# Performance work log

Measured on AMD Instinct MI355X. Metric: run time of the kernel, lower is better.

Reference implementation:

```python
import jax, jax.numpy as jnp
import numpy as np

B, N, EMB, H = 16, 1024, 128, 8
INNER = EMB * H  # 1024
EPS = 1e-5


def setup_inputs() -> dict:
    key = jax.random.key(0)
    k1, k2, k3 = jax.random.split(key, 3)
    inputs = jax.random.normal(k1, (B, N, EMB), dtype=jnp.float32)
    ln_gamma = jnp.ones((EMB,), dtype=jnp.float32)
    ln_beta = jnp.zeros((EMB,), dtype=jnp.float32)
    w_qkv = jax.random.normal(k2, (EMB, 3 * INNER), dtype=jnp.float32) * (EMB ** -0.5)
    w_proj = jax.random.normal(k3, (INNER, EMB), dtype=jnp.float32) * (INNER ** -0.5)
    b_proj = jnp.zeros((EMB,), dtype=jnp.float32)
    return {"inputs": inputs, "ln_gamma": ln_gamma, "ln_beta": ln_beta,
            "w_qkv": w_qkv, "w_proj": w_proj, "b_proj": b_proj}


def reference(inputs, ln_gamma, ln_beta, w_qkv, w_proj, b_proj):
    scale = INNER ** -0.5
    # LayerNorm over last dim
    mu = jnp.mean(inputs, axis=-1, keepdims=True)
    var = jnp.var(inputs, axis=-1, keepdims=True)
    x = (inputs - mu) * jax.lax.rsqrt(var + EPS) * ln_gamma + ln_beta
    # QKV projection (no bias)
    qkv = x @ w_qkv                                  # [b, n, 3*inner]
    q, k, v = jnp.split(qkv, 3, axis=-1)             # each [b, n, inner]
    def to_heads(a):
        return a.reshape(B, N, H, EMB).transpose(0, 2, 1, 3)  # [b, h, n, d]
    q, k, v = to_heads(q), to_heads(k), to_heads(v)
    attn = jnp.einsum('bhid,bhjd->bhij', q * scale, k)
    attn = jax.nn.softmax(attn, axis=-1)
    out = jnp.einsum('bhij,bhjd->bhid', attn, v)     # [b, h, n, d]
    out = out.transpose(0, 2, 1, 3).reshape(B, N, INNER)
    return out @ w_proj + b_proj                     # [b, n, emb]
```

## Files before the change

kernel.cpp:

```cpp
#include <hip/hip_runtime.h>
#include <hip/hip_bf16.h>


typedef __attribute__((ext_vector_type(8))) short bf16x8;
typedef __attribute__((ext_vector_type(4))) float f32x4;

__device__ __forceinline__ unsigned short f2bf(float f) {
  unsigned int u = __float_as_uint(f);
  u += 0x7FFF + ((u >> 16) & 1);
  return (unsigned short)(u >> 16);
}

__device__ __forceinline__ void gll16(const void* g, void* l) {
  __builtin_amdgcn_global_load_lds((const __attribute__((address_space(1))) unsigned int*)g,
                                   (__attribute__((address_space(3))) unsigned int*)l, 16, 0, 0);
}

__global__ __launch_bounds__(256) void k_ln(const float* __restrict__ x,
                                            const float* __restrict__ gamma,
                                            const float* __restrict__ beta,
                                            unsigned short* __restrict__ xb) {
  int row  = blockIdx.x * 4 + (threadIdx.x >> 6);
  int lane = threadIdx.x & 63;
  float2 v = *reinterpret_cast<const float2*>(x + row * 128 + lane * 2);
  float s = v.x + v.y, ss = v.x * v.x + v.y * v.y;
#pragma unroll
  for (int m = 1; m < 64; m <<= 1) { s += __shfl_xor(s, m); ss += __shfl_xor(ss, m); }
  float mu   = s * (1.0f / 128.0f);
  float var  = ss * (1.0f / 128.0f) - mu * mu;
  float rstd = rsqrtf(var + 1e-5f);
  float2 g  = *reinterpret_cast<const float2*>(gamma + lane * 2);
  float2 be = *reinterpret_cast<const float2*>(beta + lane * 2);
  ushort2 o;
  o.x = f2bf((v.x - mu) * rstd * g.x + be.x);
  o.y = f2bf((v.y - mu) * rstd * g.y + be.y);
  *reinterpret_cast<ushort2*>(xb + row * 128 + lane * 2) = o;
}

__global__ __launch_bounds__(256) void k_cast_wqkv(const float* __restrict__ w,
                                                   unsigned short* __restrict__ wt) {
  __shared__ unsigned short T[128][70];
  const int n0 = blockIdx.x * 64;
  const int tid = threadIdx.x;
#pragma unroll
  for (int i = 0; i < 32; i++) {
    int idx = i * 256 + tid;
    int k = idx >> 6, c = idx & 63;
    T[k][c] = f2bf(w[k * 3072 + n0 + c]);
  }
  __syncthreads();
#pragma unroll
  for (int i = 0; i < 32; i++) {
    int idx = i * 256 + tid;
    int n = idx >> 7, k = idx & 127;
    wt[(n0 + n) * 128 + k] = T[k][n];
  }
}

__global__ __launch_bounds__(256) void k_cast_wproj(const float* __restrict__ w,
                                                    unsigned short* __restrict__ wt) {
  __shared__ unsigned short T[128][134];
  const int k0 = blockIdx.x * 128;
  const int tid = threadIdx.x;
#pragma unroll
  for (int i = 0; i < 64; i++) {
    int idx = i * 256 + tid;
    int r = idx >> 7, c = idx & 127;
    T[r][c] = f2bf(w[(k0 + r) * 128 + c]);
  }
  __syncthreads();
#pragma unroll
  for (int i = 0; i < 64; i++) {
    int idx = i * 256 + tid;
    int c = idx >> 7, r = idx & 127;
    wt[c * 1024 + k0 + r] = T[r][c];
  }
}

__global__ __launch_bounds__(256) void k_qkv(const unsigned short* __restrict__ xb,
                                             const unsigned short* __restrict__ wt,
                                             unsigned short* __restrict__ qb,
                                             unsigned short* __restrict__ kb,
                                             unsigned short* __restrict__ vtb) {
  __shared__ __align__(16) unsigned short Xs[128][128];
  __shared__ __align__(16) unsigned short Ws[128][128];
  const int m0 = blockIdx.x * 128;
  const int n0 = blockIdx.y * 128;
  const int tid = threadIdx.x, wave = tid >> 6, lane = tid & 63;
  const int lm = lane & 15, lg = lane >> 4;
  const int wr = wave >> 1, wc = wave & 1;

#pragma unroll
  for (int ii = 0; ii < 8; ii++) {
    int row = wave * 32 + ii * 4 + (lane >> 4);
    int c = (lane & 15) ^ (row & 7);
    gll16(xb + (m0 + row) * 128 + c * 8, &Xs[wave * 32 + ii * 4][0]);
    gll16(wt + (n0 + row) * 128 + c * 8, &Ws[wave * 32 + ii * 4][0]);
  }
  __syncthreads();

  f32x4 acc[4][4];
#pragma unroll
  for (int i = 0; i < 4; i++)
#pragma unroll
    for (int j = 0; j < 4; j++) acc[i][j] = {0.f, 0.f, 0.f, 0.f};

#pragma unroll
  for (int k32 = 0; k32 < 4; k32++) {
    bf16x8 af[4], bfr[4];
#pragma unroll
    for (int mi = 0; mi < 4; mi++) {
      int row = wr * 64 + mi * 16 + lm;
      af[mi] = *(const bf16x8*)((const char*)&Xs[row][0] + ((k32 * 64 + lg * 16) ^ ((lm & 7) << 4)));
    }
#pragma unroll
    for (int ni = 0; ni < 4; ni++) {
      int row = wc * 64 + ni * 16 + lm;
      bfr[ni] = *(const bf16x8*)((const char*)&Ws[row][0] + ((k32 * 64 + lg * 16) ^ ((lm & 7) << 4)));
    }
#pragma unroll
    for (int mi = 0; mi < 4; mi++)
#pragma unroll
      for (int ni = 0; ni < 4; ni++)
        acc[mi][ni] = __builtin_amdgcn_mfma_f32_16x16x32_bf16(af[mi], bfr[ni], acc[mi][ni], 0, 0, 0);
  }

#pragma unroll
  for (int mi = 0; mi < 4; mi++)
#pragma unroll
    for (int ni = 0; ni < 4; ni++)
#pragma unroll
      for (int j = 0; j < 4; j++) {
        int m = m0 + wr * 64 + mi * 16 + 4 * (lane >> 4) + j;
        int n = n0 + wc * 64 + ni * 16 + lm;
        float val = acc[mi][ni][j];
        int bb = m >> 10, seq = m & 1023;
        int sel = n >> 10, r = n & 1023, h = r >> 7, d = r & 127;
        int bh = bb * 8 + h;
        if (sel == 0)      qb[(bh * 1024 + seq) * 128 + d] = f2bf(val * 0.04508422f);
        else if (sel == 1) kb[(bh * 1024 + seq) * 128 + d] = f2bf(val);
        else               vtb[(bh * 128 + d) * 1024 + seq] = f2bf(val);
      }
}

__global__ __launch_bounds__(256, 3) void k_flash(const unsigned short* __restrict__ qb,
                                                  const unsigned short* __restrict__ kb,
                                                  const unsigned short* __restrict__ vtb,
                                                  unsigned short* __restrict__ ob) {
  __shared__ __align__(16) unsigned short Ks[64][128];
  __shared__ __align__(16) unsigned short Vts[128][64];
  __shared__ __align__(16) unsigned short Ps[4][32][64];
  const int bi = blockIdx.x;
  const int xcd = bi & 7, g = bi >> 3;
  const int bh = xcd + 8 * (g >> 3);
  const int q0 = (g & 7) * 128;
  const int tid = threadIdx.x, wave = tid >> 6, lane = tid & 63;
  const int lm = lane & 15, lg = lane >> 4, lk8 = lg * 8;
  const int sw = (lm & 7) << 4;
  const int b = bh >> 3, h = bh & 7;

  const unsigned short* kbh = kb + bh * 131072;
  const unsigned short* vbh = vtb + bh * 131072;

  bf16x8 aq[2][4];
#pragma unroll
  for (int qs = 0; qs < 2; qs++) {
    const unsigned short* qrow = qb + (bh * 1024 + q0 + wave * 32 + qs * 16 + lm) * 128;
#pragma unroll
    for (int kc = 0; kc < 4; kc++) aq[qs][kc] = *(const bf16x8*)(qrow + kc * 32 + lk8);
  }

  f32x4 oacc[2][8];
#pragma unroll
  for (int qs = 0; qs < 2; qs++)
#pragma unroll
    for (int dt = 0; dt < 8; dt++) oacc[qs][dt] = {0.f, 0.f, 0.f, 0.f};
  float mrun[2] = {-3e38f, -3e38f}, lrun[2] = {0.f, 0.f};

  auto stage = [&](int kt) {
#pragma unroll
    for (int ii = 0; ii < 4; ii++) {
      int krow = (wave * 4 + ii) * 4 + (lane >> 4);
      int c = (lane & 15) ^ (krow & 7);
      gll16(kbh + (kt * 64 + krow) * 128 + c * 8, &Ks[(wave * 4 + ii) * 4][0]);
    }
#pragma unroll
    for (int ii = 0; ii < 4; ii++) {
      int vrow = (wave * 4 + ii) * 8 + (lane >> 3);
      int c = (lane & 7) ^ (vrow & 7);
      gll16(vbh + vrow * 1024 + kt * 64 + c * 8, &Vts[(wave * 4 + ii) * 8][0]);
    }
  };

  stage(0);
  __syncthreads();

  for (int kt = 0; kt < 16; kt++) {
    f32x4 sc[2][4];
    __builtin_amdgcn_s_setprio(1);
#pragma unroll
    for (int nt = 0; nt < 4; nt++) {
      f32x4 a0 = {0.f, 0.f, 0.f, 0.f}, a1 = {0.f, 0.f, 0.f, 0.f};
      const char* krowp = (const char*)&Ks[nt * 16 + lm][0];
#pragma unroll
      for (int kc = 0; kc < 4; kc++) {
        bf16x8 ak = *(const bf16x8*)(krowp + ((kc * 64 + lg * 16) ^ sw));
        a0 = __builtin_amdgcn_mfma_f32_16x16x32_bf16(ak, aq[0][kc], a0, 0, 0, 0);
        a1 = __builtin_amdgcn_mfma_f32_16x16x32_bf16(ak, aq[1][kc], a1, 0, 0, 0);
      }
      sc[0][nt] = a0; sc[1][nt] = a1;
    }
    __builtin_amdgcn_s_setprio(0);

#pragma unroll
    for (int qs = 0; qs < 2; qs++) {
      float mx16 = fmaxf(fmaxf(fmaxf(sc[qs][0][0], sc[qs][0][1]), fmaxf(sc[qs][0][2], sc[qs][0][3])),
                         fmaxf(fmaxf(sc[qs][1][0], sc[qs][1][1]), fmaxf(sc[qs][1][2], sc[qs][1][3])));
      mx16 = fmaxf(mx16, fmaxf(fmaxf(sc[qs][2][0], sc[qs][2][1]), fmaxf(sc[qs][2][2], sc[qs][2][3])));
      mx16 = fmaxf(mx16, fmaxf(fmaxf(sc[qs][3][0], sc[qs][3][1]), fmaxf(sc[qs][3][2], sc[qs][3][3])));
      if (!__all(mx16 <= mrun[qs] + 8.f)) {
        float mx = fmaxf(mx16, __shfl_xor(mx16, 16));
        mx = fmaxf(mx, __shfl_xor(mx, 32));
        float mnew = fmaxf(mrun[qs], mx);
        float corr = __builtin_exp2f(mrun[qs] - mnew);
        mrun[qs] = mnew;
        lrun[qs] *= corr;
#pragma unroll
        for (int dt = 0; dt < 8; dt++)
#pragma unroll
          for (int j = 0; j < 4; j++) oacc[qs][dt][j] *= corr;
      }
      float ts = 0.f;
#pragma unroll
      for (int nt = 0; nt < 4; nt++)
#pragma unroll
        for (int j = 0; j < 4; j++) {
          float e = __builtin_exp2f(sc[qs][nt][j] - mrun[qs]);
          sc[qs][nt][j] = e;
          ts += e;
        }
      lrun[qs] += ts;

      char* psrow = (char*)&Ps[wave][qs * 16 + lm][0];
#pragma unroll
      for (int nt = 0; nt < 4; nt++) {
        unsigned int w0, w1;
        asm("v_cvt_pk_bf16_f32 %0, %1, %2" : "=v"(w0) : "v"(sc[qs][nt][0]), "v"(sc[qs][nt][1]));
        asm("v_cvt_pk_bf16_f32 %0, %1, %2" : "=v"(w1) : "v"(sc[qs][nt][2]), "v"(sc[qs][nt][3]));
        int p0 = (nt * 32 + lg * 8) ^ sw;
        *(unsigned int*)(psrow + p0)     = w0;
        *(unsigned int*)(psrow + p0 + 4) = w1;
      }
    }

    __builtin_amdgcn_s_setprio(1);
#pragma unroll
    for (int t = 0; t < 2; t++) {
      bf16x8 pb0 = *(const bf16x8*)((const char*)&Ps[wave][lm][0]      + ((t * 64 + lg * 16) ^ sw));
      bf16x8 pb1 = *(const bf16x8*)((const char*)&Ps[wave][16 + lm][0] + ((t * 64 + lg * 16) ^ sw));
#pragma unroll
      for (int dt = 0; dt < 8; dt++) {
        bf16x8 av = *(const bf16x8*)((const char*)&Vts[dt * 16 + lm][0] + ((t * 64 + lg * 16) ^ sw));
        oacc[0][dt] = __builtin_amdgcn_mfma_f32_16x16x32_bf16(av, pb0, oacc[0][dt], 0, 0, 0);
        oacc[1][dt] = __builtin_amdgcn_mfma_f32_16x16x32_bf16(av, pb1, oacc[1][dt], 0, 0, 0);
      }
    }
    __builtin_amdgcn_s_setprio(0);

    __syncthreads();
    if (kt < 15) {
      stage(kt + 1);
      __syncthreads();
    }
  }

#pragma unroll
  for (int qs = 0; qs < 2; qs++) {
    float l = lrun[qs];
    l += __shfl_xor(l, 16);
    l += __shfl_xor(l, 32);
    float inv = 1.0f / l;
    unsigned short* orow = ob + ((b * 1024 + q0 + wave * 32 + qs * 16 + lm) * 8 + h) * 128;
#pragma unroll
    for (int dt = 0; dt < 8; dt++) {
#pragma unroll
      for (int pp = 0; pp < 2; pp++) {
        ushort2 o2;
        o2.x = f2bf(oacc[qs][dt][2 * pp]     * inv);
        o2.y = f2bf(oacc[qs][dt][2 * pp + 1] * inv);
        *(ushort2*)&orow[dt * 16 + 4 * lg + 2 * pp] = o2;
      }
    }
  }
}

__global__ __launch_bounds__(256) void k_proj(const unsigned short* __restrict__ ob,
                                              const unsigned short* __restrict__ wpt,
                                              const float* __restrict__ bproj,
                                              float* __restrict__ out) {
  __shared__ __align__(16) unsigned short Os[2][64][128];
  __shared__ __align__(16) unsigned short Ws2[2][128][128];
  const int m0 = blockIdx.x * 64;
  const int tid = threadIdx.x, wave = tid >> 6, lane = tid & 63;
  const int lm = lane & 15, lg = lane >> 4;
  const int wr = wave >> 1, wc = wave & 1;

  auto stage = [&](int kt, int buf) {
#pragma unroll
    for (int ii = 0; ii < 4; ii++) {
      int row = wave * 16 + ii * 4 + (lane >> 4);
      int c = (lane & 15) ^ (row & 7);
      gll16(ob + (m0 + row) * 1024 + kt * 128 + c * 8, &Os[buf][wave * 16 + ii * 4][0]);
    }
#pragma unroll
    for (int ii = 0; ii < 8; ii++) {
      int row = wave * 32 + ii * 4 + (lane >> 4);
      int c = (lane & 15) ^ (row & 7);
      gll16(wpt + row * 1024 + kt * 128 + c * 8, &Ws2[buf][wave * 32 + ii * 4][0]);
    }
  };

  f32x4 acc[2][4];
#pragma unroll
  for (int i = 0; i < 2; i++)
#pragma unroll
    for (int j = 0; j < 4; j++) acc[i][j] = {0.f, 0.f, 0.f, 0.f};

  stage(0, 0);
  __syncthreads();
  int cur = 0;

  for (int kt = 0; kt < 8; kt++) {
    if (kt < 7) stage(kt + 1, cur ^ 1);
    __builtin_amdgcn_sched_barrier(0);
#pragma unroll
    for (int k32 = 0; k32 < 4; k32++) {
      bf16x8 af[2], bfr[4];
#pragma unroll
      for (int mi = 0; mi < 2; mi++) {
        int row = wr * 32 + mi * 16 + lm;
        af[mi] = *(const bf16x8*)((const char*)&Os[cur][row][0] + ((k32 * 64 + lg * 16) ^ ((lm & 7) << 4)));
      }
#pragma unroll
      for (int ni = 0; ni < 4; ni++) {
        int row = wc * 64 + ni * 16 + lm;
        bfr[ni] = *(const bf16x8*)((const char*)&Ws2[cur][row][0] + ((k32 * 64 + lg * 16) ^ ((lm & 7) << 4)));
      }
#pragma unroll
      for (int mi = 0; mi < 2; mi++)
#pragma unroll
        for (int ni = 0; ni < 4; ni++)
          acc[mi][ni] = __builtin_amdgcn_mfma_f32_16x16x32_bf16(af[mi], bfr[ni], acc[mi][ni], 0, 0, 0);
    }
    __syncthreads();
    cur ^= 1;
  }

#pragma unroll
  for (int mi = 0; mi < 2; mi++)
#pragma unroll
    for (int ni = 0; ni < 4; ni++)
#pragma unroll
      for (int j = 0; j < 4; j++) {
        int m = m0 + wr * 32 + mi * 16 + 4 * (lane >> 4) + j;
        int n = wc * 64 + ni * 16 + lm;
        out[m * 128 + n] = acc[mi][ni][j] + bproj[n];
      }
}

extern "C" void kernel_launch(void* const* d_in, const int* in_sizes, int n_in,
                              void* d_out, int out_size, void* d_ws, size_t ws_size,
                              hipStream_t stream) {
  const float* x     = (const float*)d_in[0];
  const float* gamma = (const float*)d_in[1];
  const float* beta  = (const float*)d_in[2];
  const float* wqkv  = (const float*)d_in[3];
  const float* wproj = (const float*)d_in[4];
  const float* bproj = (const float*)d_in[5];
  float* out = (float*)d_out;

  unsigned short* ws = (unsigned short*)d_ws;
  unsigned short* xb     = ws;
  unsigned short* wqkvT  = xb + 2097152;
  unsigned short* wprojT = wqkvT + 393216;
  unsigned short* qbuf   = wprojT + 131072;
  unsigned short* kbuf   = qbuf + 16777216;
  unsigned short* vtbuf  = kbuf + 16777216;
  unsigned short* obuf   = vtbuf + 16777216;

  hipLaunchKernelGGL(k_ln,         dim3(4096),     dim3(256), 0, stream, x, gamma, beta, xb);
  hipLaunchKernelGGL(k_cast_wqkv,  dim3(48),       dim3(256), 0, stream, wqkv, wqkvT);
  hipLaunchKernelGGL(k_cast_wproj, dim3(8),        dim3(256), 0, stream, wproj, wprojT);
  hipLaunchKernelGGL(k_qkv,        dim3(128, 24),  dim3(256), 0, stream, xb, wqkvT, qbuf, kbuf, vtbuf);
  hipLaunchKernelGGL(k_flash,      dim3(1024),     dim3(256), 0, stream, qbuf, kbuf, vtbuf, obuf);
  hipLaunchKernelGGL(k_proj,       dim3(256),      dim3(256), 0, stream, obuf, wprojT, bproj, out);
}
```

Before: 187.7 us.

## Fuse prep kernels, coalesce QKV stores via LDS, widen flash per-wave query tile

Merges layernorm and both weight cast/transpose kernels into one launch to cut launch overhead. The QKV GEMM epilogue now stages results in shared memory (transposed for V) and writes contiguous rows, replacing scattered per-element stores. The flash attention kernel uses 128-thread blocks where each wave owns 64 query rows, reusing K and V fragments across four query subtiles and interleaving P conversion with PV MFMAs. This raises register pressure and lowers wave count per block.

```diff
diff --git a/kernel.cpp b/kernel.cpp
--- a/kernel.cpp
+++ b/kernel.cpp
@@ -16,64 +16,62 @@
                                    (__attribute__((address_space(3))) unsigned int*)l, 16, 0, 0);
 }
 
-__global__ __launch_bounds__(256) void k_ln(const float* __restrict__ x,
-                                            const float* __restrict__ gamma,
-                                            const float* __restrict__ beta,
-                                            unsigned short* __restrict__ xb) {
-  int row  = blockIdx.x * 4 + (threadIdx.x >> 6);
-  int lane = threadIdx.x & 63;
-  float2 v = *reinterpret_cast<const float2*>(x + row * 128 + lane * 2);
-  float s = v.x + v.y, ss = v.x * v.x + v.y * v.y;
-#pragma unroll
-  for (int m = 1; m < 64; m <<= 1) { s += __shfl_xor(s, m); ss += __shfl_xor(ss, m); }
-  float mu   = s * (1.0f / 128.0f);
-  float var  = ss * (1.0f / 128.0f) - mu * mu;
-  float rstd = rsqrtf(var + 1e-5f);
-  float2 g  = *reinterpret_cast<const float2*>(gamma + lane * 2);
-  float2 be = *reinterpret_cast<const float2*>(beta + lane * 2);
-  ushort2 o;
-  o.x = f2bf((v.x - mu) * rstd * g.x + be.x);
-  o.y = f2bf((v.y - mu) * rstd * g.y + be.y);
-  *reinterpret_cast<ushort2*>(xb + row * 128 + lane * 2) = o;
-}
-
-__global__ __launch_bounds__(256) void k_cast_wqkv(const float* __restrict__ w,
-                                                   unsigned short* __restrict__ wt) {
-  __shared__ unsigned short T[128][70];
-  const int n0 = blockIdx.x * 64;
-  const int tid = threadIdx.x;
-#pragma unroll
-  for (int i = 0; i < 32; i++) {
-    int idx = i * 256 + tid;
-    int k = idx >> 6, c = idx & 63;
-    T[k][c] = f2bf(w[k * 3072 + n0 + c]);
-  }
-  __syncthreads();
-#pragma unroll
-  for (int i = 0; i < 32; i++) {
-    int idx = i * 256 + tid;
-    int n = idx >> 7, k = idx & 127;
-    wt[(n0 + n) * 128 + k] = T[k][n];
-  }
-}
-
-__global__ __launch_bounds__(256) void k_cast_wproj(const float* __restrict__ w,
-                                                    unsigned short* __restrict__ wt) {
-  __shared__ unsigned short T[128][134];
-  const int k0 = blockIdx.x * 128;
-  const int tid = threadIdx.x;
-#pragma unroll
-  for (int i = 0; i < 64; i++) {
-    int idx = i * 256 + tid;
-    int r = idx >> 7, c = idx & 127;
-    T[r][c] = f2bf(w[(k0 + r) * 128 + c]);
-  }
-  __syncthreads();
-#pragma unroll
-  for (int i = 0; i < 64; i++) {
-    int idx = i * 256 + tid;
-    int c = idx >> 7, r = idx & 127;
-    wt[c * 1024 + k0 + r] = T[r][c];
+__global__ __launch_bounds__(256) void k_prep(const float* __restrict__ x,
+                                              const float* __restrict__ gamma,
+                                              const float* __restrict__ beta,
+                                              const float* __restrict__ wqkv,
+                                              const float* __restrict__ wproj,
+                                              unsigned short* __restrict__ xb,
+                                              unsigned short* __restrict__ wqkvT,
+                                              unsigned short* __restrict__ wprojT) {
+  __shared__ unsigned short T[17152];
+  const int bid = blockIdx.x, tid = threadIdx.x;
+  if (bid < 4096) {
+    int row  = bid * 4 + (tid >> 6);
+    int lane = tid & 63;
+    float2 v = *reinterpret_cast<const float2*>(x + row * 128 + lane * 2);
+    float s = v.x + v.y, ss = v.x * v.x + v.y * v.y;
+#pragma unroll
+    for (int m = 1; m < 64; m <<= 1) { s += __shfl_xor(s, m); ss += __shfl_xor(ss, m); }
+    float mu   = s * (1.0f / 128.0f);
+    float var  = ss * (1.0f / 128.0f) - mu * mu;
+    float rstd = rsqrtf(var + 1e-5f);
+    float2 g  = *reinterpret_cast<const float2*>(gamma + lane * 2);
+    float2 be = *reinterpret_cast<const float2*>(beta + lane * 2);
+    ushort2 o;
+    o.x = f2bf((v.x - mu) * rstd * g.x + be.x);
+    o.y = f2bf((v.y - mu) * rstd * g.y + be.y);
+    *reinterpret_cast<ushort2*>(xb + row * 128 + lane * 2) = o;
+  } else if (bid < 4144) {
+    const int n0 = (bid - 4096) * 64;
+#pragma unroll
+    for (int i = 0; i < 32; i++) {
+      int idx = i * 256 + tid;
+      int k = idx >> 6, c = idx & 63;
+      T[k * 70 + c] = f2bf(wqkv[k * 3072 + n0 + c]);
+    }
+    __syncthreads();
+#pragma unroll
+    for (int i = 0; i < 32; i++) {
+      int idx = i * 256 + tid;
+      int n = idx >> 7, k = idx & 127;
+      wqkvT[(n0 + n) * 128 + k] = T[k * 70 + n];
+    }
+  } else {
+    const int k0 = (bid - 4144) * 128;
+#pragma unroll
+    for (int i = 0; i < 64; i++) {
+      int idx = i * 256 + tid;
+      int r = idx >> 7, c = idx & 127;
+      T[r * 134 + c] = f2bf(wproj[(k0 + r) * 128 + c]);
+    }
+    __syncthreads();
+#pragma unroll
+    for (int i = 0; i < 64; i++) {
+      int idx = i * 256 + tid;
+      int c = idx >> 7, r = idx & 127;
+      wprojT[c * 1024 + k0 + r] = T[r * 134 + c];
+    }
   }
 }
 
@@ -82,8 +80,9 @@
                                              unsigned short* __restrict__ qb,
                                              unsigned short* __restrict__ kb,
                                              unsigned short* __restrict__ vtb) {
-  __shared__ __align__(16) unsigned short Xs[128][128];
-  __shared__ __align__(16) unsigned short Ws[128][128];
+  __shared__ __align__(16) unsigned short SH[32768];
+  unsigned short* Xs = SH;
+  unsigned short* Ws = SH + 16384;
   const int m0 = blockIdx.x * 128;
   const int n0 = blockIdx.y * 128;
   const int tid = threadIdx.x, wave = tid >> 6, lane = tid & 63;
@@ -94,8 +93,8 @@
   for (int ii = 0; ii < 8; ii++) {
     int row = wave * 32 + ii * 4 + (lane >> 4);
     int c = (lane & 15) ^ (row & 7);
-    gll16(xb + (m0 + row) * 128 + c * 8, &Xs[wave * 32 + ii * 4][0]);
-    gll16(wt + (n0 + row) * 128 + c * 8, &Ws[wave * 32 + ii * 4][0]);
+    gll16(xb + (m0 + row) * 128 + c * 8, Xs + (wave * 32 + ii * 4) * 128);
+    gll16(wt + (n0 + row) * 128 + c * 8, Ws + (wave * 32 + ii * 4) * 128);
   }
   __syncthreads();
 
@@ -111,12 +110,12 @@
 #pragma unroll
     for (int mi = 0; mi < 4; mi++) {
       int row = wr * 64 + mi * 16 + lm;
-      af[mi] = *(const bf16x8*)((const char*)&Xs[row][0] + ((k32 * 64 + lg * 16) ^ ((lm & 7) << 4)));
+      af[mi] = *(const bf16x8*)((const char*)(Xs + row * 128) + ((k32 * 64 + lg * 16) ^ ((lm & 7) << 4)));
     }
 #pragma unroll
     for (int ni = 0; ni < 4; ni++) {
       int row = wc * 64 + ni * 16 + lm;
-      bfr[ni] = *(const bf16x8*)((const char*)&Ws[row][0] + ((k32 * 64 + lg * 16) ^ ((lm & 7) << 4)));
+      bfr[ni] = *(const bf16x8*)((const char*)(Ws + row * 128) + ((k32 * 64 + lg * 16) ^ ((lm & 7) << 4)));
     }
 #pragma unroll
     for (int mi = 0; mi < 4; mi++)
@@ -125,31 +124,46 @@
         acc[mi][ni] = __builtin_amdgcn_mfma_f32_16x16x32_bf16(af[mi], bfr[ni], acc[mi][ni], 0, 0, 0);
   }
 
+  __syncthreads();
+  unsigned short* T = SH;
+  const int isV = (n0 >= 2048);
+  const float qscale = (n0 < 1024) ? 0.04508422f : 1.0f;
 #pragma unroll
   for (int mi = 0; mi < 4; mi++)
 #pragma unroll
     for (int ni = 0; ni < 4; ni++)
 #pragma unroll
       for (int j = 0; j < 4; j++) {
-        int m = m0 + wr * 64 + mi * 16 + 4 * (lane >> 4) + j;
-        int n = n0 + wc * 64 + ni * 16 + lm;
-        float val = acc[mi][ni][j];
-        int bb = m >> 10, seq = m & 1023;
-        int sel = n >> 10, r = n & 1023, h = r >> 7, d = r & 127;
-        int bh = bb * 8 + h;
-        if (sel == 0)      qb[(bh * 1024 + seq) * 128 + d] = f2bf(val * 0.04508422f);
-        else if (sel == 1) kb[(bh * 1024 + seq) * 128 + d] = f2bf(val);
-        else               vtb[(bh * 128 + d) * 1024 + seq] = f2bf(val);
-      }
-}
-
-__global__ __launch_bounds__(256, 3) void k_flash(const unsigned short* __restrict__ qb,
-                                                  const unsigned short* __restrict__ kb,
-                                                  const unsigned short* __restrict__ vtb,
-                                                  unsigned short* __restrict__ ob) {
+        int mloc = wr * 64 + mi * 16 + 4 * lg + j;
+        int nloc = wc * 64 + ni * 16 + lm;
+        unsigned short v = f2bf(acc[mi][ni][j] * qscale);
+        if (isV) T[nloc * 136 + mloc] = v;
+        else     T[mloc * 136 + nloc] = v;
+      }
+  __syncthreads();
+  const int bb = m0 >> 10, seq0 = m0 & 1023;
+  const int hh = (n0 & 1023) >> 7;
+  const int bh = bb * 8 + hh;
+  unsigned short* outp; int rstride;
+  if (n0 < 1024)      { outp = qb + (bh * 1024 + seq0) * 128; rstride = 128; }
+  else if (n0 < 2048) { outp = kb + (bh * 1024 + seq0) * 128; rstride = 128; }
+  else                { outp = vtb + bh * 131072 + seq0;      rstride = 1024; }
+#pragma unroll
+  for (int i = 0; i < 32; i++) {
+    int flat = i * 512 + tid * 2;
+    int row = flat >> 7, c = flat & 127;
+    ushort2 v2 = *(ushort2*)&T[row * 136 + c];
+    *(ushort2*)(outp + row * rstride + c) = v2;
+  }
+}
+
+__global__ __launch_bounds__(128) void k_flash(const unsigned short* __restrict__ qb,
+                                               const unsigned short* __restrict__ kb,
+                                               const unsigned short* __restrict__ vtb,
+                                               unsigned short* __restrict__ ob) {
   __shared__ __align__(16) unsigned short Ks[64][128];
   __shared__ __align__(16) unsigned short Vts[128][64];
-  __shared__ __align__(16) unsigned short Ps[4][32][64];
+  __shared__ __align__(16) unsigned short Ps[2][64][32];
   const int bi = blockIdx.x;
   const int xcd = bi & 7, g = bi >> 3;
   const int bh = xcd + 8 * (g >> 3);
@@ -157,38 +171,40 @@
   const int tid = threadIdx.x, wave = tid >> 6, lane = tid & 63;
   const int lm = lane & 15, lg = lane >> 4, lk8 = lg * 8;
   const int sw = (lm & 7) << 4;
+  const int psw = (lm >> 1) & 3;
   const int b = bh >> 3, h = bh & 7;
 
   const unsigned short* kbh = kb + bh * 131072;
   const unsigned short* vbh = vtb + bh * 131072;
 
-  bf16x8 aq[2][4];
-#pragma unroll
-  for (int qs = 0; qs < 2; qs++) {
-    const unsigned short* qrow = qb + (bh * 1024 + q0 + wave * 32 + qs * 16 + lm) * 128;
+  bf16x8 aq[4][4];
+#pragma unroll
+  for (int qs = 0; qs < 4; qs++) {
+    const unsigned short* qrow = qb + (bh * 1024 + q0 + wave * 64 + qs * 16 + lm) * 128;
 #pragma unroll
     for (int kc = 0; kc < 4; kc++) aq[qs][kc] = *(const bf16x8*)(qrow + kc * 32 + lk8);
   }
 
-  f32x4 oacc[2][8];
-#pragma unroll
-  for (int qs = 0; qs < 2; qs++)
+  f32x4 oacc[4][8];
+#pragma unroll
+  for (int qs = 0; qs < 4; qs++)
 #pragma unroll
     for (int dt = 0; dt < 8; dt++) oacc[qs][dt] = {0.f, 0.f, 0.f, 0.f};
-  float mrun[2] = {-3e38f, -3e38f}, lrun[2] = {0.f, 0.f};
+  float mrun[4] = {0.f, 0.f, 0.f, 0.f};
+  float lrun[4] = {0.f, 0.f, 0.f, 0.f};
 
   auto stage = [&](int kt) {
 #pragma unroll
-    for (int ii = 0; ii < 4; ii++) {
-      int krow = (wave * 4 + ii) * 4 + (lane >> 4);
+    for (int ii = 0; ii < 8; ii++) {
+      int krow = wave * 32 + ii * 4 + (lane >> 4);
       int c = (lane & 15) ^ (krow & 7);
-      gll16(kbh + (kt * 64 + krow) * 128 + c * 8, &Ks[(wave * 4 + ii) * 4][0]);
-    }
-#pragma unroll
-    for (int ii = 0; ii < 4; ii++) {
-      int vrow = (wave * 4 + ii) * 8 + (lane >> 3);
+      gll16(kbh + (kt * 64 + krow) * 128 + c * 8, &Ks[wave * 32 + ii * 4][0]);
+    }
+#pragma unroll
+    for (int ii = 0; ii < 8; ii++) {
+      int vrow = wave * 64 + ii * 8 + (lane >> 3);
       int c = (lane & 7) ^ (vrow & 7);
-      gll16(vbh + vrow * 1024 + kt * 64 + c * 8, &Vts[(wave * 4 + ii) * 8][0]);
+      gll16(vbh + vrow * 1024 + kt * 64 + c * 8, &Vts[wave * 64 + ii * 8][0]);
     }
   };
 
@@ -196,24 +212,27 @@
   __syncthreads();
 
   for (int kt = 0; kt < 16; kt++) {
-    f32x4 sc[2][4];
+    f32x4 sc[4][4];
     __builtin_amdgcn_s_setprio(1);
 #pragma unroll
     for (int nt = 0; nt < 4; nt++) {
-      f32x4 a0 = {0.f, 0.f, 0.f, 0.f}, a1 = {0.f, 0.f, 0.f, 0.f};
       const char* krowp = (const char*)&Ks[nt * 16 + lm][0];
-#pragma unroll
-      for (int kc = 0; kc < 4; kc++) {
-        bf16x8 ak = *(const bf16x8*)(krowp + ((kc * 64 + lg * 16) ^ sw));
-        a0 = __builtin_amdgcn_mfma_f32_16x16x32_bf16(ak, aq[0][kc], a0, 0, 0, 0);
-        a1 = __builtin_amdgcn_mfma_f32_16x16x32_bf16(ak, aq[1][kc], a1, 0, 0, 0);
-      }
-      sc[0][nt] = a0; sc[1][nt] = a1;
+      bf16x8 ak[4];
+#pragma unroll
+      for (int kc = 0; kc < 4; kc++) ak[kc] = *(const bf16x8*)(krowp + ((kc * 64 + lg * 16) ^ sw));
+#pragma unroll
+      for (int qs = 0; qs < 4; qs++) {
+        f32x4 a = {0.f, 0.f, 0.f, 0.f};
+#pragma unroll
+        for (int kc = 0; kc < 4; kc++)
+          a = __builtin_amdgcn_mfma_f32_16x16x32_bf16(ak[kc], aq[qs][kc], a, 0, 0, 0);
+        sc[qs][nt] = a;
+      }
     }
     __builtin_amdgcn_s_setprio(0);
 
 #pragma unroll
-    for (int qs = 0; qs < 2; qs++) {
+    for (int qs = 0; qs < 4; qs++) {
       float mx16 = fmaxf(fmaxf(fmaxf(sc[qs][0][0], sc[qs][0][1]), fmaxf(sc[qs][0][2], sc[qs][0][3])),
                          fmaxf(fmaxf(sc[qs][1][0], sc[qs][1][1]), fmaxf(sc[qs][1][2], sc[qs][1][3])));
       mx16 = fmaxf(mx16, fmaxf(fmaxf(sc[qs][2][0], sc[qs][2][1]), fmaxf(sc[qs][2][2], sc[qs][2][3])));
@@ -230,42 +249,49 @@
 #pragma unroll
           for (int j = 0; j < 4; j++) oacc[qs][dt][j] *= corr;
       }
-      float ts = 0.f;
-#pragma unroll
-      for (int nt = 0; nt < 4; nt++)
+    }
+
+    float ts[4] = {0.f, 0.f, 0.f, 0.f};
+#pragma unroll
+    for (int t = 0; t < 2; t++) {
+#pragma unroll
+      for (int qs = 0; qs < 4; qs++) {
+        float e[8];
 #pragma unroll
         for (int j = 0; j < 4; j++) {
-          float e = __builtin_exp2f(sc[qs][nt][j] - mrun[qs]);
-          sc[qs][nt][j] = e;
-          ts += e;
+          e[j]     = __builtin_exp2f(sc[qs][2 * t][j]     - mrun[qs]);
+          e[4 + j] = __builtin_exp2f(sc[qs][2 * t + 1][j] - mrun[qs]);
+          ts[qs] += e[j] + e[4 + j];
         }
-      lrun[qs] += ts;
-
-      char* psrow = (char*)&Ps[wave][qs * 16 + lm][0];
-#pragma unroll
-      for (int nt = 0; nt < 4; nt++) {
-        unsigned int w0, w1;
-        asm("v_cvt_pk_bf16_f32 %0, %1, %2" : "=v"(w0) : "v"(sc[qs][nt][0]), "v"(sc[qs][nt][1]));
-        asm("v_cvt_pk_bf16_f32 %0, %1, %2" : "=v"(w1) : "v"(sc[qs][nt][2]), "v"(sc[qs][nt][3]));
-        int p0 = (nt * 32 + lg * 8) ^ sw;
-        *(unsigned int*)(psrow + p0)     = w0;
-        *(unsigned int*)(psrow + p0 + 4) = w1;
-      }
-    }
-
-    __builtin_amdgcn_s_setprio(1);
-#pragma unroll
-    for (int t = 0; t < 2; t++) {
-      bf16x8 pb0 = *(const bf16x8*)((const char*)&Ps[wave][lm][0]      + ((t * 64 + lg * 16) ^ sw));
-      bf16x8 pb1 = *(const bf16x8*)((const char*)&Ps[wave][16 + lm][0] + ((t * 64 + lg * 16) ^ sw));
+        unsigned int w0, w1, w2, w3;
+        asm("v_cvt_pk_bf16_f32 %0, %1, %2" : "=v"(w0) : "v"(e[0]), "v"(e[1]));
+        asm("v_cvt_pk_bf16_f32 %0, %1, %2" : "=v"(w1) : "v"(e[2]), "v"(e[3]));
+        asm("v_cvt_pk_bf16_f32 %0, %1, %2" : "=v"(w2) : "v"(e[4]), "v"(e[5]));
+        asm("v_cvt_pk_bf16_f32 %0, %1, %2" : "=v"(w3) : "v"(e[6]), "v"(e[7]));
+        char* psrow = (char*)&Ps[wave][qs * 16 + lm][0];
+        int s0 = (((lg >> 1)    ) ^ psw) * 16 + (lg & 1) * 8;
+        int s1 = (((lg >> 1) + 2) ^ psw) * 16 + (lg & 1) * 8;
+        *(unsigned int*)(psrow + s0)     = w0;
+        *(unsigned int*)(psrow + s0 + 4) = w1;
+        *(unsigned int*)(psrow + s1)     = w2;
+        *(unsigned int*)(psrow + s1 + 4) = w3;
+      }
+      bf16x8 pb[4];
+#pragma unroll
+      for (int qs = 0; qs < 4; qs++)
+        pb[qs] = *(const bf16x8*)((const char*)&Ps[wave][qs * 16 + lm][0] + 16 * (lg ^ psw));
+      __builtin_amdgcn_s_setprio(1);
 #pragma unroll
       for (int dt = 0; dt < 8; dt++) {
         bf16x8 av = *(const bf16x8*)((const char*)&Vts[dt * 16 + lm][0] + ((t * 64 + lg * 16) ^ sw));
-        oacc[0][dt] = __builtin_amdgcn_mfma_f32_16x16x32_bf16(av, pb0, oacc[0][dt], 0, 0, 0);
-        oacc[1][dt] = __builtin_amdgcn_mfma_f32_16x16x32_bf16(av, pb1, oacc[1][dt], 0, 0, 0);
-      }
-    }
-    __builtin_amdgcn_s_setprio(0);
+#pragma unroll
+        for (int qs = 0; qs < 4; qs++)
+          oacc[qs][dt] = __builtin_amdgcn_mfma_f32_16x16x32_bf16(av, pb[qs], oacc[qs][dt], 0, 0, 0);
+      }
+      __builtin_amdgcn_s_setprio(0);
+    }
+#pragma unroll
+    for (int qs = 0; qs < 4; qs++) lrun[qs] += ts[qs];
 
     __syncthreads();
     if (kt < 15) {
@@ -275,12 +301,12 @@
   }
 
 #pragma unroll
-  for (int qs = 0; qs < 2; qs++) {
+  for (int qs = 0; qs < 4; qs++) {
     float l = lrun[qs];
     l += __shfl_xor(l, 16);
     l += __shfl_xor(l, 32);
     float inv = 1.0f / l;
-    unsigned short* orow = ob + ((b * 1024 + q0 + wave * 32 + qs * 16 + lm) * 8 + h) * 128;
+    unsigned short* orow = ob + ((b * 1024 + q0 + wave * 64 + qs * 16 + lm) * 8 + h) * 128;
 #pragma unroll
     for (int dt = 0; dt < 8; dt++) {
 #pragma unroll
@@ -388,10 +414,8 @@
   unsigned short* vtbuf  = kbuf + 16777216;
   unsigned short* obuf   = vtbuf + 16777216;
 
-  hipLaunchKernelGGL(k_ln,         dim3(4096),     dim3(256), 0, stream, x, gamma, beta, xb);
-  hipLaunchKernelGGL(k_cast_wqkv,  dim3(48),       dim3(256), 0, stream, wqkv, wqkvT);
-  hipLaunchKernelGGL(k_cast_wproj, dim3(8),        dim3(256), 0, stream, wproj, wprojT);
-  hipLaunchKernelGGL(k_qkv,        dim3(128, 24),  dim3(256), 0, stream, xb, wqkvT, qbuf, kbuf, vtbuf);
-  hipLaunchKernelGGL(k_flash,      dim3(1024),     dim3(256), 0, stream, qbuf, kbuf, vtbuf, obuf);
-  hipLaunchKernelGGL(k_proj,       dim3(256),      dim3(256), 0, stream, obuf, wprojT, bproj, out);
-}
+  hipLaunchKernelGGL(k_prep, dim3(4152),    dim3(256), 0, stream, x, gamma, beta, wqkv, wproj, xb, wqkvT, wprojT);
+  hipLaunchKernelGGL(k_qkv,  dim3(128, 24), dim3(256), 0, stream, xb, wqkvT, qbuf, kbuf, vtbuf);
+  hipLaunchKernelGGL(k_flash, dim3(1024),   dim3(128), 0, stream, qbuf, kbuf, vtbuf, obuf);
+  hipLaunchKernelGGL(k_proj, dim3(256),     dim3(256), 0, stream, obuf, wprojT, bproj, out);
+}
```

Measured after the change: 203.3 us. 1.08x slower.
